# Performance work log

Hardware: AMD Instinct MI355X
Metric: run time of the kernel (lower is better)

The kernel has to match this reference:

```python
import jax, jax.numpy as jnp
import numpy as np

T, B, H = 512, 128, 512

def setup_inputs() -> dict:
    key = jax.random.key(0)
    k1, k2, k3, k4 = jax.random.split(key, 4)
    s = 1.0 / np.sqrt(H)
    x = jax.random.normal(k1, (T, B, H), dtype=jnp.float32)
    resets = jax.random.randint(k2, (T, B), 0, 2).astype(bool)
    Wi = jax.random.normal(k3, (H, 3 * H), dtype=jnp.float32) * s
    bi = jnp.zeros((3 * H,), dtype=jnp.float32)
    Wh = jax.random.normal(k4, (H, 3 * H), dtype=jnp.float32) * s
    bhn = jnp.zeros((H,), dtype=jnp.float32)
    h0 = jnp.zeros((B, H), dtype=jnp.float32)
    return {"x": x, "resets": resets, "Wi": Wi, "bi": bi, "Wh": Wh, "bhn": bhn, "h0": h0}

def reference(x, resets, Wi, bi, Wh, bhn, h0):
    # Scanned flax GRUCell with per-step carry reset (reset -> zeros carry).
    def step(h, inp):
        xt, rt = inp                                   # xt: [B,H], rt: [B]
        h = jnp.where(rt[:, None], jnp.zeros_like(h), h)
        gi = xt @ Wi + bi                              # [B,3H]
        gh = h @ Wh                                    # [B,3H]
        ir, iz, inn = jnp.split(gi, 3, axis=-1)
        hr, hz, hn = jnp.split(gh, 3, axis=-1)
        r = jax.nn.sigmoid(ir + hr)
        z = jax.nn.sigmoid(iz + hz)
        n = jnp.tanh(inn + r * (hn + bhn))             # bias only on h 'n' gate (flax GRUCell)
        new_h = (1.0 - z) * n + z * h
        return new_h, new_h
    _, ys = jax.lax.scan(step, h0, (x, resets))
    return ys                                          # [T,B,H]
```

## Files before the change

### kernel.cpp

```cpp
#include <hip/hip_runtime.h>


typedef _Float16 f16;
typedef _Float16 f16x8 __attribute__((ext_vector_type(8)));
typedef float f32x4 __attribute__((ext_vector_type(4)));
typedef float f32x16 __attribute__((ext_vector_type(16)));

#define TT 512
#define BB 128
#define HH 512
#define H3 1536
#define TBR 65536
#define NC 64
#define CL 8
#define NR 8192
static const size_t PL = (size_t)TBR * HH;

__device__ __forceinline__ float sigf(float x) { return 1.f / (1.f + __expf(-x)); }

__global__ __launch_bounds__(256) void k_prep(
    const float* __restrict__ Wi, const float* __restrict__ Wh,
    const int* __restrict__ resets,
    f16* __restrict__ WiT, f16* __restrict__ WhT,
    int* __restrict__ fr, int* __restrict__ cnt) {
  int idx = blockIdx.x * 256 + threadIdx.x;
  if (idx < HH * H3) {
    int n = idx >> 9;
    int k = idx & (HH - 1);
    WiT[idx] = (f16)Wi[(size_t)k * H3 + n];
    WhT[idx] = (f16)Wh[(size_t)k * H3 + n];
  }
  if (idx < NR) {
    int c = idx >> 7, b = idx & 127;
    int f = CL;
    for (int s = CL - 1; s >= 0; --s)
      if (resets[(c * CL + s) * BB + b]) f = s;
    fr[idx] = f;
    atomicAdd(&cnt[f], 1);
  }
}

__global__ void k_sort(int* __restrict__ cnt) {
  int st = 0;
  cnt[16 + 8] = 0;
  for (int f = 7; f >= 0; --f) {
    st += cnt[f + 1];
    cnt[16 + f] = st;
  }
  for (int f = 1; f <= 8; ++f) cnt[32 + f] = cnt[16 + f];
}

__global__ __launch_bounds__(256) void k_scatter(
    const int* __restrict__ fr, int* __restrict__ cnt, int* __restrict__ list) {
  int idx = blockIdx.x * 256 + threadIdx.x;
  if (idx < NR) {
    int f = fr[idx];
    if (f >= 1) {
      int pos = atomicAdd(&cnt[32 + f], 1);
      list[pos] = idx;
    }
  }
}

__global__ __launch_bounds__(256) void k_gemm_gi(
    const float* __restrict__ x, const f16* __restrict__ WiT,
    const float* __restrict__ bi, f16* __restrict__ gi) {
  __shared__ __align__(16) f16 xs[64 * 512];
  const int tid = threadIdx.x;
  const int lane = tid & 63;
  const int w = tid >> 6;
  const size_t i0 = (size_t)blockIdx.x * 64;

  {
    const int row = tid >> 2;
    const int mi = row >> 5;
    const int lin = (row & 31) + ((tid & 1) << 5);
    const int koct = (tid & 3) * 8;
#pragma unroll 4
    for (int kb32 = 0; kb32 < 16; ++kb32) {
      const int k = kb32 * 32 + koct;
      const float* xp = x + (i0 + row) * HH + k;
      float4 v0 = *(const float4*)xp;
      float4 v1 = *(const float4*)(xp + 4);
      f16x8 a8;
      a8[0] = (f16)v0.x; a8[1] = (f16)v0.y; a8[2] = (f16)v0.z; a8[3] = (f16)v0.w;
      a8[4] = (f16)v1.x; a8[5] = (f16)v1.y; a8[6] = (f16)v1.z; a8[7] = (f16)v1.w;
      *(f16x8*)&xs[((k >> 4) * 2 + mi) * 512 + lin * 8] = a8;
    }
  }
  __syncthreads();

  const int ln31 = lane & 31;
  const int kh8 = (lane >> 5) * 8;
  const int r4 = (lane >> 5) * 4;

  for (int jt = 0; jt < 6; ++jt) {
    const int j0 = jt * 256 + w * 64;
    f32x16 acc[2][2] = {};
    const f16* bp0 = WiT + (size_t)(j0 + ln31) * HH + kh8;
    const f16* bp1 = bp0 + (size_t)32 * HH;
#pragma unroll 4
    for (int kb = 0; kb < 32; ++kb) {
      f16x8 af0 = *(const f16x8*)&xs[(kb * 2 + 0) * 512 + lane * 8];
      f16x8 af1 = *(const f16x8*)&xs[(kb * 2 + 1) * 512 + lane * 8];
      f16x8 bf0 = *(const f16x8*)(bp0 + kb * 16);
      f16x8 bf1 = *(const f16x8*)(bp1 + kb * 16);
      acc[0][0] = __builtin_amdgcn_mfma_f32_32x32x16_f16(af0, bf0, acc[0][0], 0, 0, 0);
      acc[0][1] = __builtin_amdgcn_mfma_f32_32x32x16_f16(af0, bf1, acc[0][1], 0, 0, 0);
      acc[1][0] = __builtin_amdgcn_mfma_f32_32x32x16_f16(af1, bf0, acc[1][0], 0, 0, 0);
      acc[1][1] = __builtin_amdgcn_mfma_f32_32x32x16_f16(af1, bf1, acc[1][1], 0, 0, 0);
    }
#pragma unroll
    for (int ni = 0; ni < 2; ++ni) {
      const int j = j0 + ni * 32 + ln31;
      const float bj = bi[j];
      const int p = j >> 9, jj = j & 511;
#pragma unroll
      for (int mi = 0; mi < 2; ++mi)
#pragma unroll
        for (int r = 0; r < 16; ++r) {
          const int row = mi * 32 + (r & 3) + 8 * (r >> 2) + r4;
          gi[(size_t)p * PL + (i0 + row) * HH + jj] =
              (f16)(acc[mi][ni][r] + bj);
        }
    }
  }
}

__global__ __launch_bounds__(256) void k_step0(
    const int* __restrict__ resets, const f16* __restrict__ gi,
    const float* __restrict__ bhn, float* __restrict__ out,
    f16* __restrict__ hA) {
  int gid = blockIdx.x * 256 + threadIdx.x;
  int row = gid >> 6;
  int c8 = (gid & 63) * 8;
  int c = row >> 7, b = row & 127;
  size_t girow = (size_t)c * 1024 + b;
  const f16x8 g0 = *(const f16x8*)(gi + girow * HH + c8);
  const f16x8 g1 = *(const f16x8*)(gi + PL + girow * HH + c8);
  const f16x8 g2 = *(const f16x8*)(gi + 2 * PL + girow * HH + c8);
  const int z1 = resets[(c * CL + 1) * BB + b];
  float4 o[2];
  f16x8 hn;
#pragma unroll
  for (int u = 0; u < 8; ++u) {
    float r = sigf((float)g0[u]);
    float z = sigf((float)g1[u]);
    float n = tanhf((float)g2[u] + r * bhn[c8 + u]);
    float h = (1.f - z) * n;
    ((float*)o)[u] = h;
    hn[u] = z1 ? (f16)0.f : (f16)h;
  }
  *(float4*)(out + girow * HH + c8) = o[0];
  *(float4*)(out + girow * HH + c8 + 4) = o[1];
  *(f16x8*)(hA + (size_t)row * HH + c8) = hn;
}

__global__ __launch_bounds__(256, 2) void k_phase1(
    int s, const int* __restrict__ resets, const f16* __restrict__ WhT,
    const f16* __restrict__ gi, const float* __restrict__ bhn,
    float* __restrict__ out, const f16* __restrict__ hrd,
    f16* __restrict__ hwr) {
  __shared__ __align__(16) f16 As[128 * 40];
  __shared__ __align__(16) f16 Bs[192 * 40];
  const int tid = threadIdx.x;
  const int lane = tid & 63;
  const int w = tid >> 6;
  const int c = blockIdx.x;
  const int j0 = blockIdx.y * 64;
  const int t = c * CL + s;
  const int wm = (w & 1) * 64;
  const int wn = (w >> 1) * 32;
  const int fr = lane & 15;
  const int q8 = (lane >> 4) * 8;

  f32x4 acc[3][4][2] = {};

  for (int kb = 0; kb < 16; ++kb) {
    const int k0 = kb * 32;
#pragma unroll
    for (int uu = 0; uu < 2; ++uu) {
      int u = tid + uu * 256;
      int row = u >> 2, oc = (u & 3) * 8;
      *(f16x8*)&As[row * 40 + oc] =
          *(const f16x8*)(hrd + ((size_t)(c * BB + row)) * HH + k0 + oc);
    }
#pragma unroll
    for (int uu = 0; uu < 3; ++uu) {
      int u = tid + uu * 256;
      int row = u >> 2, oc = (u & 3) * 8;
      int g = row >> 6, j = j0 + (row & 63);
      *(f16x8*)&Bs[row * 40 + oc] =
          *(const f16x8*)(WhT + ((size_t)(g * HH + j)) * HH + k0 + oc);
    }
    __syncthreads();
    f16x8 af[4];
#pragma unroll
    for (int mi = 0; mi < 4; ++mi)
      af[mi] = *(const f16x8*)&As[(wm + mi * 16 + fr) * 40 + q8];
    f16x8 bf[3][2];
#pragma unroll
    for (int g = 0; g < 3; ++g)
#pragma unroll
      for (int ni = 0; ni < 2; ++ni)
        bf[g][ni] = *(const f16x8*)&Bs[(g * 64 + wn + ni * 16 + fr) * 40 + q8];
#pragma unroll
    for (int g = 0; g < 3; ++g)
#pragma unroll
      for (int mi = 0; mi < 4; ++mi)
#pragma unroll
        for (int ni = 0; ni < 2; ++ni)
          acc[g][mi][ni] = __builtin_amdgcn_mfma_f32_16x16x32_f16(
              af[mi], bf[g][ni], acc[g][mi][ni], 0, 0, 0);
    __syncthreads();
  }

  const int trow = (lane >> 4) * 4;
#pragma unroll
  for (int mi = 0; mi < 4; ++mi)
#pragma unroll
    for (int ni = 0; ni < 2; ++ni) {
      const int j = j0 + wn + ni * 16 + fr;
      const float bh = bhn[j];
#pragma unroll
      for (int r = 0; r < 4; ++r) {
        const int b = wm + mi * 16 + trow + r;
        const size_t girow = (size_t)c * 1024 + (size_t)s * BB + b;
        const float gr = (float)gi[girow * HH + j];
        const float gz = (float)gi[PL + girow * HH + j];
        const float gn = (float)gi[2 * PL + girow * HH + j];
        const float hp = (float)hrd[((size_t)(c * BB + b)) * HH + j];
        const float rr = sigf(gr + acc[0][mi][ni][r]);
        const float zz = sigf(gz + acc[1][mi][ni][r]);
        const float nn = tanhf(gn + rr * (acc[2][mi][ni][r] + bh));
        const float hnew = (1.f - zz) * nn + zz * hp;
        out[girow * HH + j] = hnew;
        int zr = (s < 7) ? resets[(t + 1) * BB + b] : 0;
        hwr[((size_t)(c * BB + b)) * HH + j] = zr ? (f16)0.f : (f16)hnew;
      }
    }
}

__global__ __launch_bounds__(256) void k_bound(
    const int* __restrict__ fr, const f16* __restrict__ hend,
    const float* __restrict__ h0, f16* __restrict__ hin) {
  int gid = blockIdx.x * 256 + threadIdx.x;
  int row = gid >> 6;
  int o8 = (gid & 63) * 8;
  int c = row >> 7, b = row & 127;
  if (c == 0) {
    const float* hp = h0 + (size_t)b * HH + o8;
    float4 v0 = *(const float4*)hp;
    float4 v1 = *(const float4*)(hp + 4);
    f16x8 h;
    h[0] = (f16)v0.x; h[1] = (f16)v0.y; h[2] = (f16)v0.z; h[3] = (f16)v0.w;
    h[4] = (f16)v1.x; h[5] = (f16)v1.y; h[6] = (f16)v1.z; h[7] = (f16)v1.w;
    *(f16x8*)(hin + (size_t)row * HH + o8) = h;
  } else if (fr[row - BB] < CL) {
    *(f16x8*)(hin + (size_t)row * HH + o8) =
        *(const f16x8*)(hend + (size_t)(row - BB) * HH + o8);
  }
}

__global__ __launch_bounds__(1024) void k_chain(
    const int* __restrict__ fr, const f16* __restrict__ hend,
    const f16* __restrict__ WhT, const f16* __restrict__ gi,
    const float* __restrict__ bhn, const float* __restrict__ h0,
    f16* __restrict__ hin) {
  const int row0 = blockIdx.x;
  const int c0 = row0 >> 7, b = row0 & 127;
  if (fr[row0] != CL) return;
  if (c0 > 0 && fr[row0 - BB] == CL) return;
  if (c0 == NC - 1) return;

  __shared__ float hs[HH];
  __shared__ float gh[H3];
  __shared__ float part[8 * H3];
  const int tid = threadIdx.x;
  const int lane = tid & 63;
  const int w = tid >> 6;
  if (c0 == 0) {
    for (int i = tid; i < HH; i += 1024) hs[i] = h0[(size_t)b * HH + i];
  } else {
    for (int i = tid; i < HH; i += 1024)
      hs[i] = (float)hend[(size_t)(row0 - BB) * HH + i];
  }
  __syncthreads();

  int c = c0;
  while (c < NC - 1) {
    for (int s = 0; s < CL; ++s) {
      const size_t girow = (size_t)(c * CL + s) * BB + b;
      float gr_v = 0.f, gz_v = 0.f, gn_v = 0.f, hp_v = 0.f, bh_v = 0.f;
      if (tid < HH) {
        gr_v = (float)gi[girow * HH + tid];
        gz_v = (float)gi[PL + girow * HH + tid];
        gn_v = (float)gi[2 * PL + girow * HH + tid];
        bh_v = bhn[tid];
        hp_v = hs[tid];
      }
      float hv[8];
      {
        float4 h0v = *(const float4*)&hs[lane * 8];
        float4 h1v = *(const float4*)&hs[lane * 8 + 4];
        hv[0] = h0v.x; hv[1] = h0v.y; hv[2] = h0v.z; hv[3] = h0v.w;
        hv[4] = h1v.x; hv[5] = h1v.y; hv[6] = h1v.z; hv[7] = h1v.w;
      }
      const f16* wp = WhT + (size_t)(w * 96) * HH + lane * 8;
#pragma unroll 8
      for (int r = 0; r < 96; ++r) {
        f16x8 wv = *(const f16x8*)(wp + (size_t)r * HH);
        float a = 0.f;
#pragma unroll
        for (int u = 0; u < 8; ++u) a += (float)wv[u] * hv[u];
        a += __shfl_xor(a, 32, 64);
        a += __shfl_xor(a, 16, 64);
        a += __shfl_xor(a, 8, 64);
        if (lane < 8) part[lane * H3 + (w * 96 + r)] = a;
      }
      __syncthreads();
      for (int n = tid; n < H3; n += 1024) {
        float a = part[n];
#pragma unroll
        for (int u = 1; u < 8; ++u) a += part[u * H3 + n];
        gh[n] = a;
      }
      __syncthreads();
      if (tid < HH) {
        const int j = tid;
        const float rr = sigf(gr_v + gh[j]);
        const float zz = sigf(gz_v + gh[HH + j]);
        const float nn = tanhf(gn_v + rr * (gh[2 * HH + j] + bh_v));
        hs[j] = (1.f - zz) * nn + zz * hp_v;
      }
      __syncthreads();
    }
    const int nrow = (c + 1) * BB + b;
    for (int i = tid; i < HH; i += 1024)
      hin[(size_t)nrow * HH + i] = (f16)hs[i];
    if (fr[nrow] != CL) break;
    ++c;
  }
}

__global__ __launch_bounds__(256) void k_phase3(
    int s, const int* __restrict__ cnt, const int* __restrict__ list,
    const f16* __restrict__ WhT, const f16* __restrict__ gi,
    const float* __restrict__ bhn, float* __restrict__ out,
    f16* __restrict__ hph) {
  const int count = cnt[16 + s];
  const int r0 = blockIdx.x * 16;
  if (r0 >= count) return;
  __shared__ __align__(16) f16 As[16 * 520];
  __shared__ int rows[16];
  const int tid = threadIdx.x;
  const int lane = tid & 63;
  const int w = tid >> 6;
  if (tid < 16) rows[tid] = (r0 + tid < count) ? list[r0 + tid] : -1;
  __syncthreads();
#pragma unroll
  for (int uu = 0; uu < 4; ++uu) {
    int u = tid + uu * 256;
    int row = u >> 6, oc = (u & 63) * 8;
    int rid = rows[row];
    f16x8 v = {};
    if (rid >= 0) v = *(const f16x8*)(hph + (size_t)rid * HH + oc);
    *(f16x8*)&As[row * 520 + oc] = v;
  }
  __syncthreads();
  const int fr16 = lane & 15;
  const int q8 = (lane >> 4) * 8;
  const int trow = (lane >> 4) * 4;
  for (int jt = 0; jt < 8; ++jt) {
    const int jb = w * 128 + jt * 16;
    f32x4 a0 = {}, a1 = {}, a2 = {};
#pragma unroll 4
    for (int kb = 0; kb < 16; ++kb) {
      const int k0 = kb * 32;
      f16x8 af = *(const f16x8*)&As[fr16 * 520 + k0 + q8];
      f16x8 b0 = *(const f16x8*)(WhT + ((size_t)(jb + fr16)) * HH + k0 + q8);
      f16x8 b1 = *(const f16x8*)(WhT + ((size_t)(HH + jb + fr16)) * HH + k0 + q8);
      f16x8 b2 = *(const f16x8*)(WhT + ((size_t)(2 * HH + jb + fr16)) * HH + k0 + q8);
      a0 = __builtin_amdgcn_mfma_f32_16x16x32_f16(af, b0, a0, 0, 0, 0);
      a1 = __builtin_amdgcn_mfma_f32_16x16x32_f16(af, b1, a1, 0, 0, 0);
      a2 = __builtin_amdgcn_mfma_f32_16x16x32_f16(af, b2, a2, 0, 0, 0);
    }
    const int j = jb + fr16;
    const float bh = bhn[j];
#pragma unroll
    for (int r = 0; r < 4; ++r) {
      const int rid = rows[trow + r];
      if (rid < 0) continue;
      const int c = rid >> 7, b = rid & 127;
      const size_t girow = (size_t)(c * CL + s) * BB + b;
      const float gr = (float)gi[girow * HH + j];
      const float gz = (float)gi[PL + girow * HH + j];
      const float gn = (float)gi[2 * PL + girow * HH + j];
      const float hp = (float)hph[(size_t)rid * HH + j];
      const float rr = sigf(gr + a0[r]);
      const float zz = sigf(gz + a1[r]);
      const float nn = tanhf(gn + rr * (a2[r] + bh));
      const float hnew = (1.f - zz) * nn + zz * hp;
      out[girow * HH + j] = hnew;
      hph[(size_t)rid * HH + j] = (f16)hnew;
    }
  }
}

extern "C" void kernel_launch(void* const* d_in, const int* in_sizes, int n_in,
                              void* d_out, int out_size, void* d_ws, size_t ws_size,
                              hipStream_t stream) {
  const float* x = (const float*)d_in[0];
  const int* resets = (const int*)d_in[1];
  const float* Wi = (const float*)d_in[2];
  const float* bi = (const float*)d_in[3];
  const float* Wh = (const float*)d_in[4];
  const float* bhn = (const float*)d_in[5];
  const float* h0 = (const float*)d_in[6];
  float* out = (float*)d_out;

  char* ws = (char*)d_ws;
  size_t off = 0;
  f16* gi = (f16*)(ws + off);   off += 3 * PL * sizeof(f16);
  f16* WiT = (f16*)(ws + off);  off += (size_t)HH * H3 * sizeof(f16);
  f16* WhT = (f16*)(ws + off);  off += (size_t)HH * H3 * sizeof(f16);
  f16* hA = (f16*)(ws + off);   off += (size_t)NR * HH * sizeof(f16);
  f16* hB = (f16*)(ws + off);   off += (size_t)NR * HH * sizeof(f16);
  f16* hin = (f16*)(ws + off);  off += (size_t)NR * HH * sizeof(f16);
  int* fr = (int*)(ws + off);   off += NR * sizeof(int);
  int* list = (int*)(ws + off); off += NR * sizeof(int);
  int* cnt = (int*)(ws + off);  off += 64 * sizeof(int);
  (void)ws_size; (void)in_sizes; (void)n_in; (void)out_size;

  hipMemsetAsync(cnt, 0, 64 * sizeof(int), stream);
  k_prep<<<dim3(3072), 256, 0, stream>>>(Wi, Wh, resets, WiT, WhT, fr, cnt);
  k_sort<<<dim3(1), 1, 0, stream>>>(cnt);
  k_scatter<<<dim3(32), 256, 0, stream>>>(fr, cnt, list);
  k_gemm_gi<<<dim3(TBR / 64), 256, 0, stream>>>(x, WiT, bi, gi);
  k_step0<<<dim3(NR * 64 / 256), 256, 0, stream>>>(resets, gi, bhn, out, hA);
  for (int s = 1; s < CL; ++s) {
    const f16* hrd = (s & 1) ? hA : hB;
    f16* hwr = (s & 1) ? hB : hA;
    k_phase1<<<dim3(NC, 8), 256, 0, stream>>>(s, resets, WhT, gi, bhn, out, hrd, hwr);
  }
  k_bound<<<dim3(NR * 64 / 256), 256, 0, stream>>>(fr, hB, h0, hin);
  k_chain<<<dim3(NR), 1024, 0, stream>>>(fr, hB, WhT, gi, bhn, h0, hin);
  for (int s = 0; s < CL; ++s)
    k_phase3<<<dim3(NR / 16), 256, 0, stream>>>(s, cnt, list, WhT, gi, bhn, out, hin);
}
```

Measured before the change: 1.848 ms.

## Batch reset-free chain rows into MFMA tiles in a persistent chain kernel

Replaces the per-row chain kernel, which used scalar dot products and shuffle reductions, with a kernel that gathers up to 32 chain-start rows into a shared f16 tile. Each recurrent step is then computed with 32x32x16 MFMA over a pre-swizzled copy of Wh. Chain-start rows are compacted into a list during scatter, so a few persistent blocks handle them instead of launching one block per row. This adds a weight re-layout kernel and extra workspace, and it lowers parallelism when few chains exist.

```diff
diff --git a/kernel.cpp b/kernel.cpp
--- a/kernel.cpp
+++ b/kernel.cpp
@@ -40,6 +40,17 @@
   }
 }
 
+__global__ __launch_bounds__(256) void k_prepB(
+    const f16* __restrict__ WhT, f16* __restrict__ WhTf) {
+  int u = blockIdx.x * 256 + threadIdx.x;
+  int l = u & 63;
+  int kb = (u >> 6) & 31;
+  int t = u >> 11;
+  f16x8 v = *(const f16x8*)(WhT + (size_t)(t * 32 + (l & 31)) * HH +
+                            kb * 16 + (l >> 5) * 8);
+  *(f16x8*)(WhTf + (size_t)u * 8) = v;
+}
+
 __global__ void k_sort(int* __restrict__ cnt) {
   int st = 0;
   cnt[16 + 8] = 0;
@@ -51,13 +62,19 @@
 }
 
 __global__ __launch_bounds__(256) void k_scatter(
-    const int* __restrict__ fr, int* __restrict__ cnt, int* __restrict__ list) {
+    const int* __restrict__ fr, int* __restrict__ cnt, int* __restrict__ list,
+    int* __restrict__ slist) {
   int idx = blockIdx.x * 256 + threadIdx.x;
   if (idx < NR) {
     int f = fr[idx];
     if (f >= 1) {
       int pos = atomicAdd(&cnt[32 + f], 1);
       list[pos] = idx;
+    }
+    int c = idx >> 7;
+    if (f == CL && c < NC - 1 && (c == 0 || fr[idx - BB] < CL)) {
+      int p = atomicAdd(&cnt[48], 1);
+      slist[p] = idx;
     }
   }
 }
@@ -262,84 +279,115 @@
   }
 }
 
-__global__ __launch_bounds__(1024) void k_chain(
+__global__ __launch_bounds__(1024) void k_chain2(
     const int* __restrict__ fr, const f16* __restrict__ hend,
-    const f16* __restrict__ WhT, const f16* __restrict__ gi,
+    const f16* __restrict__ WhTf, const f16* __restrict__ gi,
     const float* __restrict__ bhn, const float* __restrict__ h0,
-    f16* __restrict__ hin) {
-  const int row0 = blockIdx.x;
-  const int c0 = row0 >> 7, b = row0 & 127;
-  if (fr[row0] != CL) return;
-  if (c0 > 0 && fr[row0 - BB] == CL) return;
-  if (c0 == NC - 1) return;
-
-  __shared__ float hs[HH];
-  __shared__ float gh[H3];
-  __shared__ float part[8 * H3];
+    f16* __restrict__ hin, const int* __restrict__ slist,
+    const int* __restrict__ cnt) {
+  const int count = cnt[48];
+  const int nbat = (count + 31) >> 5;
+  __shared__ __align__(16) f16 hsA[32 * 512];
+  __shared__ int ch[32];
+  __shared__ int anyact;
   const int tid = threadIdx.x;
   const int lane = tid & 63;
   const int w = tid >> 6;
-  if (c0 == 0) {
-    for (int i = tid; i < HH; i += 1024) hs[i] = h0[(size_t)b * HH + i];
-  } else {
-    for (int i = tid; i < HH; i += 1024)
-      hs[i] = (float)hend[(size_t)(row0 - BB) * HH + i];
-  }
-  __syncthreads();
-
-  int c = c0;
-  while (c < NC - 1) {
-    for (int s = 0; s < CL; ++s) {
-      const size_t girow = (size_t)(c * CL + s) * BB + b;
-      float gr_v = 0.f, gz_v = 0.f, gn_v = 0.f, hp_v = 0.f, bh_v = 0.f;
-      if (tid < HH) {
-        gr_v = (float)gi[girow * HH + tid];
-        gz_v = (float)gi[PL + girow * HH + tid];
-        gn_v = (float)gi[2 * PL + girow * HH + tid];
-        bh_v = bhn[tid];
-        hp_v = hs[tid];
+  const int nc = lane & 31;
+  const int hi = lane >> 5;
+
+  for (int bat = blockIdx.x; bat < nbat; bat += gridDim.x) {
+    if (tid < 32) {
+      int r = bat * 32 + tid;
+      ch[tid] = (r < count) ? slist[r] : -1;
+    }
+    __syncthreads();
+    for (int u = tid; u < 32 * 64; u += 1024) {
+      int m = u >> 6, o8 = (u & 63) * 8;
+      int cr = ch[m];
+      f16x8 h = {};
+      if (cr >= 0) {
+        if ((cr >> 7) == 0) {
+          const float* hp = h0 + (size_t)(cr & 127) * HH + o8;
+          float4 v0 = *(const float4*)hp;
+          float4 v1 = *(const float4*)(hp + 4);
+          h[0] = (f16)v0.x; h[1] = (f16)v0.y; h[2] = (f16)v0.z; h[3] = (f16)v0.w;
+          h[4] = (f16)v1.x; h[5] = (f16)v1.y; h[6] = (f16)v1.z; h[7] = (f16)v1.w;
+        } else {
+          h = *(const f16x8*)(hend + (size_t)(cr - BB) * HH + o8);
+        }
       }
-      float hv[8];
-      {
-        float4 h0v = *(const float4*)&hs[lane * 8];
-        float4 h1v = *(const float4*)&hs[lane * 8 + 4];
-        hv[0] = h0v.x; hv[1] = h0v.y; hv[2] = h0v.z; hv[3] = h0v.w;
-        hv[4] = h1v.x; hv[5] = h1v.y; hv[6] = h1v.z; hv[7] = h1v.w;
+      *(f16x8*)&hsA[(o8 >> 4) * 512 + (m + ((o8 >> 3) & 1) * 32) * 8] = h;
+    }
+    __syncthreads();
+
+    while (true) {
+      for (int s = 0; s < CL; ++s) {
+        f32x16 a0 = {}, a1 = {}, a2 = {};
+        const f16* b0p = WhTf + ((size_t)(w)*32 * 64 + lane) * 8;
+        const f16* b1p = WhTf + ((size_t)(16 + w) * 32 * 64 + lane) * 8;
+        const f16* b2p = WhTf + ((size_t)(32 + w) * 32 * 64 + lane) * 8;
+#pragma unroll 4
+        for (int kb = 0; kb < 32; ++kb) {
+          f16x8 af = *(const f16x8*)&hsA[kb * 512 + lane * 8];
+          f16x8 bf0 = *(const f16x8*)(b0p + (size_t)kb * 512);
+          f16x8 bf1 = *(const f16x8*)(b1p + (size_t)kb * 512);
+          f16x8 bf2 = *(const f16x8*)(b2p + (size_t)kb * 512);
+          a0 = __builtin_amdgcn_mfma_f32_32x32x16_f16(af, bf0, a0, 0, 0, 0);
+          a1 = __builtin_amdgcn_mfma_f32_32x32x16_f16(af, bf1, a1, 0, 0, 0);
+          a2 = __builtin_amdgcn_mfma_f32_32x32x16_f16(af, bf2, a2, 0, 0, 0);
+        }
+        __syncthreads();
+        const int j = w * 32 + nc;
+        const float bh = bhn[j];
+#pragma unroll
+        for (int r = 0; r < 16; ++r) {
+          const int m = (r & 3) + 8 * (r >> 2) + 4 * hi;
+          const int cr = ch[m];
+          const size_t girow =
+              (cr >= 0)
+                  ? ((size_t)(cr >> 7) * 1024 + (size_t)s * BB + (cr & 127))
+                  : 0;
+          const float gr = (float)gi[girow * HH + j];
+          const float gz = (float)gi[PL + girow * HH + j];
+          const float gn = (float)gi[2 * PL + girow * HH + j];
+          const int ha =
+              (j >> 4) * 512 + (m + ((j >> 3) & 1) * 32) * 8 + (j & 7);
+          const float hp = (float)hsA[ha];
+          const float rr = sigf(gr + a0[r]);
+          const float zz = sigf(gz + a1[r]);
+          const float nn = tanhf(gn + rr * (a2[r] + bh));
+          hsA[ha] = (f16)((1.f - zz) * nn + zz * hp);
+        }
+        __syncthreads();
       }
-      const f16* wp = WhT + (size_t)(w * 96) * HH + lane * 8;
-#pragma unroll 8
-      for (int r = 0; r < 96; ++r) {
-        f16x8 wv = *(const f16x8*)(wp + (size_t)r * HH);
-        float a = 0.f;
-#pragma unroll
-        for (int u = 0; u < 8; ++u) a += (float)wv[u] * hv[u];
-        a += __shfl_xor(a, 32, 64);
-        a += __shfl_xor(a, 16, 64);
-        a += __shfl_xor(a, 8, 64);
-        if (lane < 8) part[lane * H3 + (w * 96 + r)] = a;
+      for (int u = tid; u < 32 * 64; u += 1024) {
+        int m = u >> 6, o8 = (u & 63) * 8;
+        int cr = ch[m];
+        if (cr >= 0) {
+          f16x8 h = *(const f16x8*)&hsA[(o8 >> 4) * 512 +
+                                        (m + ((o8 >> 3) & 1) * 32) * 8];
+          *(f16x8*)(hin + (size_t)(cr + BB) * HH + o8) = h;
+        }
+      }
+      if (tid == 0) anyact = 0;
+      __syncthreads();
+      if (tid < 32) {
+        int cr = ch[tid];
+        if (cr >= 0) {
+          int nrow = cr + BB;
+          if (fr[nrow] == CL && (nrow >> 7) < NC - 1) {
+            ch[tid] = nrow;
+            atomicAdd(&anyact, 1);
+          } else {
+            ch[tid] = -1;
+          }
+        }
       }
       __syncthreads();
-      for (int n = tid; n < H3; n += 1024) {
-        float a = part[n];
-#pragma unroll
-        for (int u = 1; u < 8; ++u) a += part[u * H3 + n];
-        gh[n] = a;
-      }
-      __syncthreads();
-      if (tid < HH) {
-        const int j = tid;
-        const float rr = sigf(gr_v + gh[j]);
-        const float zz = sigf(gz_v + gh[HH + j]);
-        const float nn = tanhf(gn_v + rr * (gh[2 * HH + j] + bh_v));
-        hs[j] = (1.f - zz) * nn + zz * hp_v;
-      }
-      __syncthreads();
-    }
-    const int nrow = (c + 1) * BB + b;
-    for (int i = tid; i < HH; i += 1024)
-      hin[(size_t)nrow * HH + i] = (f16)hs[i];
-    if (fr[nrow] != CL) break;
-    ++c;
+      if (anyact == 0) break;
+    }
+    __syncthreads();
   }
 }
 
@@ -421,21 +469,24 @@
 
   char* ws = (char*)d_ws;
   size_t off = 0;
-  f16* gi = (f16*)(ws + off);   off += 3 * PL * sizeof(f16);
-  f16* WiT = (f16*)(ws + off);  off += (size_t)HH * H3 * sizeof(f16);
-  f16* WhT = (f16*)(ws + off);  off += (size_t)HH * H3 * sizeof(f16);
-  f16* hA = (f16*)(ws + off);   off += (size_t)NR * HH * sizeof(f16);
-  f16* hB = (f16*)(ws + off);   off += (size_t)NR * HH * sizeof(f16);
-  f16* hin = (f16*)(ws + off);  off += (size_t)NR * HH * sizeof(f16);
-  int* fr = (int*)(ws + off);   off += NR * sizeof(int);
-  int* list = (int*)(ws + off); off += NR * sizeof(int);
-  int* cnt = (int*)(ws + off);  off += 64 * sizeof(int);
+  f16* gi = (f16*)(ws + off);    off += 3 * PL * sizeof(f16);
+  f16* WiT = (f16*)(ws + off);   off += (size_t)HH * H3 * sizeof(f16);
+  f16* WhT = (f16*)(ws + off);   off += (size_t)HH * H3 * sizeof(f16);
+  f16* WhTf = (f16*)(ws + off);  off += (size_t)HH * H3 * sizeof(f16);
+  f16* hA = (f16*)(ws + off);    off += (size_t)NR * HH * sizeof(f16);
+  f16* hB = (f16*)(ws + off);    off += (size_t)NR * HH * sizeof(f16);
+  f16* hin = (f16*)(ws + off);   off += (size_t)NR * HH * sizeof(f16);
+  int* fr = (int*)(ws + off);    off += NR * sizeof(int);
+  int* list = (int*)(ws + off);  off += NR * sizeof(int);
+  int* slist = (int*)(ws + off); off += NR * sizeof(int);
+  int* cnt = (int*)(ws + off);   off += 64 * sizeof(int);
   (void)ws_size; (void)in_sizes; (void)n_in; (void)out_size;
 
   hipMemsetAsync(cnt, 0, 64 * sizeof(int), stream);
   k_prep<<<dim3(3072), 256, 0, stream>>>(Wi, Wh, resets, WiT, WhT, fr, cnt);
+  k_prepB<<<dim3(384), 256, 0, stream>>>(WhT, WhTf);
   k_sort<<<dim3(1), 1, 0, stream>>>(cnt);
-  k_scatter<<<dim3(32), 256, 0, stream>>>(fr, cnt, list);
+  k_scatter<<<dim3(32), 256, 0, stream>>>(fr, cnt, list, slist);
   k_gemm_gi<<<dim3(TBR / 64), 256, 0, stream>>>(x, WiT, bi, gi);
   k_step0<<<dim3(NR * 64 / 256), 256, 0, stream>>>(resets, gi, bhn, out, hA);
   for (int s = 1; s < CL; ++s) {
@@ -444,7 +495,7 @@
     k_phase1<<<dim3(NC, 8), 256, 0, stream>>>(s, resets, WhT, gi, bhn, out, hrd, hwr);
   }
   k_bound<<<dim3(NR * 64 / 256), 256, 0, stream>>>(fr, hB, h0, hin);
-  k_chain<<<dim3(NR), 1024, 0, stream>>>(fr, hB, WhT, gi, bhn, h0, hin);
+  k_chain2<<<dim3(4), 1024, 0, stream>>>(fr, hB, WhTf, gi, bhn, h0, hin, slist, cnt);
   for (int s = 0; s < CL; ++s)
     k_phase3<<<dim3(NR / 16), 256, 0, stream>>>(s, cnt, list, WhT, gi, bhn, out, hin);
 }
```

After: 1.813 ms. Within noise of the previous version (-1.9%).
